# Kernel optimization log

Hardware: AMD Instinct MI355X
Metric: run time of the kernel (lower is better)

## Reference

```python
import jax, jax.numpy as jnp
import numpy as np

RADIUS = 0.005
MAX_DEGREE = 32
N = 65536
S = 2048
INPUT_DIM = 32
HIDDEN = 256
NDIM = 1  # code requires ndim==1 for the add of pos-embed to projection


def sincos_embed(pos, dim):
    # pos: [N, ndim]; output [N, ndim*dim] (== [N, dim] for ndim=1), as in source
    half = dim // 2
    freq = jnp.exp(jnp.arange(half, dtype=pos.dtype) * (-jnp.log(10000.0) / (half - 1)))
    e = pos[:, :, None] * freq[None, None, :]          # [N, ndim, half]
    e = jnp.concatenate([jnp.sin(e), jnp.cos(e)], -1)  # [N, ndim, dim]
    return e.reshape(pos.shape[0], -1)


def setup_inputs() -> dict:
    key = jax.random.key(0)
    ks = jax.random.split(key, 8)
    inp = {
        "input_feat": jax.random.normal(ks[0], (N, INPUT_DIM), jnp.float32),
        "input_pos": jax.random.uniform(ks[1], (N, NDIM), jnp.float32),
        "supernode_idxs": jnp.arange(S, dtype=jnp.int32),
        "batch_idx": jnp.zeros((N,), jnp.int32),
        # LinearProjection (input proj), lecun_normal-like init
        "proj_W": jax.random.normal(ks[2], (INPUT_DIM, HIDDEN), jnp.float32) / np.sqrt(INPUT_DIM),
        "proj_b": jnp.zeros((HIDDEN,), jnp.float32),
        # message MLP: Dense(2H->H), gelu, Dense(H->H)
        "msg_W1": jax.random.normal(ks[3], (2 * HIDDEN, HIDDEN), jnp.float32) / np.sqrt(2 * HIDDEN),
        "msg_b1": jnp.zeros((HIDDEN,), jnp.float32),
        "msg_W2": jax.random.normal(ks[4], (HIDDEN, HIDDEN), jnp.float32) / np.sqrt(HIDDEN),
        "msg_b2": jnp.zeros((HIDDEN,), jnp.float32),
    }
    return inp


def reference(input_feat, input_pos, supernode_idxs, batch_idx,
              proj_W, proj_b, msg_W1, msg_b1, msg_W2, msg_b2):
    # node embedding: linear projection + continuous sincos positional embed
    x = input_feat @ proj_W + proj_b + sincos_embed(input_pos, HIDDEN)  # [N, H]

    # radius graph restricted to edges whose dst is a supernode:
    # per supernode, take up to MAX_DEGREE nearest neighbors within RADIUS (self-loop allowed)
    sup_pos = input_pos[supernode_idxs]                                  # [S, ndim]
    d2 = jnp.sum((sup_pos[:, None, :] - input_pos[None, :, :]) ** 2, -1)  # [S, N]
    neg_d2, nbr = jax.lax.top_k(-d2, MAX_DEGREE)                          # [S, K]
    within = (-neg_d2) <= RADIUS * RADIUS                                 # [S, K] mask

    x_src = x[nbr]                                                        # [S, K, H]
    x_dst = jnp.broadcast_to(x[supernode_idxs][:, None, :], x_src.shape) # [S, K, H]
    m_in = jnp.concatenate([x_src, x_dst], axis=-1)                       # [S, K, 2H]
    h = jax.nn.gelu(m_in @ msg_W1 + msg_b1)
    m = h @ msg_W2 + msg_b2                                               # [S, K, H]

    # segment mean over each supernode's in-radius edges
    w = within[..., None].astype(m.dtype)
    pooled = jnp.sum(m * w, axis=1) / jnp.maximum(jnp.sum(w, axis=1), 1.0)  # [S, H]
    return pooled[None]  # [batch_size=1, S, H]
```

## Files before the change

### kernel.cpp

```cpp
#include <hip/hip_runtime.h>
#include <hip/hip_bf16.h>
#include <float.h>

#define N_NODES 65536
#define S_SUP   2048
#define HDIM    256
#define KNN     32
#define NBINS   4096
#define CAP     4096
#define GSUP    4

typedef __attribute__((ext_vector_type(8))) __bf16 bf16x8;
typedef __attribute__((ext_vector_type(4))) float  f32x4;

__global__ __launch_bounds__(256) void embed_kernel(
        const float* __restrict__ feat, const float* __restrict__ pos,
        const float* __restrict__ W, const float* __restrict__ b,
        __hip_bfloat16* __restrict__ xb) {
    __shared__ float sf[64][32];
    __shared__ float sp[64];
    int tid = threadIdx.x;
    int rb = blockIdx.x * 64;
    {
        int r = tid >> 2, kg = tid & 3;
        const float* src = feat + (size_t)(rb + r) * 32 + kg * 8;
        float4 v0 = *(const float4*)(src);
        float4 v1 = *(const float4*)(src + 4);
        *(float4*)&sf[r][kg * 8]     = v0;
        *(float4*)&sf[r][kg * 8 + 4] = v1;
    }
    if (tid < 64) sp[tid] = pos[rb + tid];
    int c = tid;
    float wcol[32];
#pragma unroll
    for (int k = 0; k < 32; ++k) wcol[k] = W[k * 256 + c];
    float bias = b[c];
    const float coef = -logf(10000.0f) / 127.0f;
    float fr = expf((float)(c & 127) * coef);
    bool is_sin = (c < 128);
    __syncthreads();
    for (int r = 0; r < 64; ++r) {
        float acc = bias;
#pragma unroll
        for (int k = 0; k < 32; ++k) acc = fmaf(sf[r][k], wcol[k], acc);
        float e = sp[r] * fr;
        acc += is_sin ? __sinf(e) : __cosf(e);
        xb[(size_t)(rb + r) * 256 + c] = __float2bfloat16(acc);
    }
}

__global__ void transpose_w1_kernel(const float* __restrict__ W1, __hip_bfloat16* __restrict__ w1t) {
    int k = blockIdx.x;
    int n = threadIdx.x;
    w1t[(size_t)n * 512 + k] = __float2bfloat16(W1[(size_t)k * 256 + n]);
}

__device__ __forceinline__ int pos_bin(float p) {
    int b = (int)(p * (float)NBINS);
    return min(max(b, 0), NBINS - 1);
}

__global__ void hist_kernel(const float* __restrict__ pos, int* __restrict__ bin_cnt) {
    int n = blockIdx.x * blockDim.x + threadIdx.x;
    atomicAdd(&bin_cnt[pos_bin(pos[n])], 1);
}

__global__ void scan_kernel(const int* __restrict__ bin_cnt, int* __restrict__ bin_ofs,
                            int* __restrict__ cursor) {
    __shared__ int sdata[1024];
    int t = threadIdx.x;
    int v[4]; int s = 0;
#pragma unroll
    for (int i = 0; i < 4; ++i) { v[i] = bin_cnt[t * 4 + i]; s += v[i]; }
    sdata[t] = s;
    __syncthreads();
    for (int off = 1; off < 1024; off <<= 1) {
        int add = (t >= off) ? sdata[t - off] : 0;
        __syncthreads();
        sdata[t] += add;
        __syncthreads();
    }
    int run = sdata[t] - s;
#pragma unroll
    for (int i = 0; i < 4; ++i) {
        bin_ofs[t * 4 + i] = run;
        cursor[t * 4 + i]  = run;
        run += v[i];
    }
    if (t == 1023) bin_ofs[NBINS] = run;
}

__global__ void scatter_kernel(const float* __restrict__ pos, int* __restrict__ cursor,
                               int* __restrict__ sidx, float* __restrict__ spos) {
    int n = blockIdx.x * blockDim.x + threadIdx.x;
    float p = pos[n];
    int b = pos_bin(p);
    int dst = atomicAdd(&cursor[b], 1);
    sidx[dst] = n;
    spos[dst] = p;
}

__global__ void topk_kernel(const float* __restrict__ pos, const int* __restrict__ sup,
                            const int* __restrict__ bin_ofs, const int* __restrict__ sidx,
                            const float* __restrict__ spos,
                            int* __restrict__ nbr, int* __restrict__ within,
                            int* __restrict__ ncnt) {
    __shared__ float cd2[CAP];
    __shared__ int   cidx[CAP];
    __shared__ float rd2[KNN];
    __shared__ int   ridx[KNN];
    int s = blockIdx.x;
    int lane = threadIdx.x;
    float p = pos[sup[s]];
    int hb = pos_bin(p);
    const float BINW = 1.0f / (float)NBINS;
    int ccnt = 0;
    for (int r = 2;; r <<= 1) {
        int lo = max(hb - r, 0), hi = min(hb + r, NBINS - 1);
        int start = bin_ofs[lo], end = bin_ofs[hi + 1];
        ccnt = min(end - start, CAP);
        for (int i = lane; i < ccnt; i += 64) {
            float pp = spos[start + i];
            float d = p - pp;
            cd2[i] = d * d;
            cidx[i] = sidx[start + i];
        }
        __syncthreads();
        float gl = (lo == 0) ? FLT_MAX : (p - (float)lo * BINW);
        float gr = (hi == NBINS - 1) ? FLT_MAX : ((float)(hi + 1) * BINW - p);
        float g = fminf(gl, gr);
        float g2 = (g >= FLT_MAX) ? FLT_MAX : (g * 0.999f) * (g * 0.999f);
        int cw = 0;
        for (int i = lane; i < ccnt; i += 64) cw += (cd2[i] < g2) ? 1 : 0;
        for (int o = 32; o; o >>= 1) cw += __shfl_xor(cw, o);
        if (cw >= KNN || (lo == 0 && hi == NBINS - 1)) break;
        __syncthreads();
    }
    for (int t = 0; t < KNN; ++t) {
        unsigned long long best = ~0ULL;
        int bslot = -1;
        for (int i = lane; i < ccnt; i += 64) {
            unsigned long long k =
                ((unsigned long long)__float_as_uint(cd2[i]) << 32) | (unsigned)cidx[i];
            if (k < best) { best = k; bslot = i; }
        }
        unsigned long long mybest = best;
        for (int o = 32; o; o >>= 1) {
            unsigned long long other = __shfl_xor(best, o);
            best = best < other ? best : other;
        }
        if (mybest == best && bslot >= 0) cd2[bslot] = FLT_MAX;
        if (lane == 0) {
            rd2[t]  = __uint_as_float((unsigned)(best >> 32));
            ridx[t] = (int)(unsigned)(best & 0xffffffffULL);
        }
        __syncthreads();
    }
    const float R2 = (float)(0.005 * 0.005);
    if (lane < KNN) {
        float d2v = rd2[lane];
        int w = (d2v <= R2) ? 1 : 0;
        nbr[s * KNN + lane] = ridx[lane];
        within[s * KNN + lane] = w;
        unsigned long long m = __ballot(w != 0);
        int cnt = __popcll(m & 0xffffffffULL);
        if (lane == 0) ncnt[s] = cnt;
    }
}

__device__ __forceinline__ float gelu_tanh(float v) {
    float v3 = v * v * v;
    float t = tanhf(0.7978845608028654f * (v + 0.044715f * v3));
    return 0.5f * v * (1.0f + t);
}

__global__ __launch_bounds__(256) void edge_mlp_pool_kernel(
        const __hip_bfloat16* __restrict__ xb_,
        const __hip_bfloat16* __restrict__ w1t_,
        const float* __restrict__ b1,
        const int* __restrict__ sup,
        const int* __restrict__ nbr, const int* __restrict__ within,
        const int* __restrict__ ncnt, float* __restrict__ mh) {
    const ushort* xb  = (const ushort*)xb_;
    const ushort* w1t = (const ushort*)w1t_;
    int s0 = blockIdx.x * GSUP;
    int tid = threadIdx.x;
    int l = tid & 63, w = tid >> 6;
    int lr = l & 15, lg = l >> 4;
    __shared__ int snbr[GSUP][KNN];
    __shared__ int swin[GSUP][KNN];
    __shared__ int ssup[GSUP];
    if (tid < GSUP * KNN) {
        int g = tid >> 5, j = tid & 31;
        snbr[g][j] = nbr[(s0 + g) * KNN + j];
        swin[g][j] = within[(s0 + g) * KNN + j];
    }
    if (tid < GSUP) ssup[tid] = sup[s0 + tid];
    __syncthreads();
    const ushort* ar0[GSUP];
    const ushort* ar1[GSUP];
    const ushort* asp[GSUP];
#pragma unroll
    for (int g = 0; g < GSUP; ++g) {
        ar0[g] = xb + (size_t)snbr[g][lr]      * 256;
        ar1[g] = xb + (size_t)snbr[g][16 + lr] * 256;
        asp[g] = xb + (size_t)ssup[g]          * 256;
    }
    const ushort* bbase = w1t + (size_t)(w * 64 + lr) * 512;
    int koff = lg * 8;
    f32x4 acc[GSUP][2][4] = {};
#pragma unroll 1
    for (int ks = 0; ks < 8; ++ks) {
        int k = ks * 32 + koff;
        bf16x8 bfr[4];
#pragma unroll
        for (int nt = 0; nt < 4; ++nt) bfr[nt] = *(const bf16x8*)(bbase + (size_t)nt * 16 * 512 + k);
#pragma unroll
        for (int g = 0; g < GSUP; ++g) {
            bf16x8 a0 = *(const bf16x8*)(ar0[g] + k);
            bf16x8 a1 = *(const bf16x8*)(ar1[g] + k);
#pragma unroll
            for (int nt = 0; nt < 4; ++nt) {
                acc[g][0][nt] = __builtin_amdgcn_mfma_f32_16x16x32_bf16(a0, bfr[nt], acc[g][0][nt], 0, 0, 0);
                acc[g][1][nt] = __builtin_amdgcn_mfma_f32_16x16x32_bf16(a1, bfr[nt], acc[g][1][nt], 0, 0, 0);
            }
        }
    }
#pragma unroll 1
    for (int ks = 0; ks < 8; ++ks) {
        int k = ks * 32 + koff;
        bf16x8 bfr[4];
#pragma unroll
        for (int nt = 0; nt < 4; ++nt) bfr[nt] = *(const bf16x8*)(bbase + (size_t)nt * 16 * 512 + 256 + k);
#pragma unroll
        for (int g = 0; g < GSUP; ++g) {
            bf16x8 a = *(const bf16x8*)(asp[g] + k);
#pragma unroll
            for (int nt = 0; nt < 4; ++nt) {
                acc[g][0][nt] = __builtin_amdgcn_mfma_f32_16x16x32_bf16(a, bfr[nt], acc[g][0][nt], 0, 0, 0);
                acc[g][1][nt] = __builtin_amdgcn_mfma_f32_16x16x32_bf16(a, bfr[nt], acc[g][1][nt], 0, 0, 0);
            }
        }
    }
#pragma unroll
    for (int nt = 0; nt < 4; ++nt) {
        int col = w * 64 + nt * 16 + lr;
        float bb = b1[col];
#pragma unroll
        for (int g = 0; g < GSUP; ++g) {
            float msum = 0.f;
#pragma unroll
            for (int mt = 0; mt < 2; ++mt)
#pragma unroll
                for (int d = 0; d < 4; ++d) {
                    int row = mt * 16 + lg * 4 + d;
                    float v = acc[g][mt][nt][d] + bb;
                    float gl = gelu_tanh(v);
                    msum += swin[g][row] ? gl : 0.f;
                }
            msum += __shfl_xor(msum, 16);
            msum += __shfl_xor(msum, 32);
            if (lg == 0) {
                float inv = 1.0f / (float)max(ncnt[s0 + g], 1);
                mh[(size_t)(s0 + g) * 256 + col] = msum * inv;
            }
        }
    }
}

__global__ void gemm64_kernel(const float* __restrict__ A, const int* __restrict__ rowidx,
                              const float* __restrict__ B, const float* __restrict__ bias,
                              const int* __restrict__ ncnt, float* __restrict__ C, int ldc) {
    __shared__ float At[32][68];
    __shared__ float Bs[32][64];
    int tid = threadIdx.x;
    int rb = blockIdx.x * 64, cb = blockIdx.y * 64;
    int tx = tid & 15, ty = tid >> 4;
    float acc[4][4] = {};
    int lr = tid >> 2, kg = tid & 3;
    int arow = rowidx ? rowidx[rb + lr] : (rb + lr);
    const float* aptr = A + (size_t)arow * 256 + kg * 8;
    int k2 = tid >> 3, cg = tid & 7;
    const float* bptr = B + (size_t)k2 * 256 + cb + cg * 8;
    for (int kc = 0; kc < 256; kc += 32) {
        float4 a0 = *(const float4*)(aptr + kc);
        float4 a1 = *(const float4*)(aptr + kc + 4);
        float4 b0 = *(const float4*)(bptr + (size_t)kc * 256);
        float4 b1v = *(const float4*)(bptr + (size_t)kc * 256 + 4);
        At[kg * 8 + 0][lr] = a0.x; At[kg * 8 + 1][lr] = a0.y;
        At[kg * 8 + 2][lr] = a0.z; At[kg * 8 + 3][lr] = a0.w;
        At[kg * 8 + 4][lr] = a1.x; At[kg * 8 + 5][lr] = a1.y;
        At[kg * 8 + 6][lr] = a1.z; At[kg * 8 + 7][lr] = a1.w;
        *(float4*)&Bs[k2][cg * 8]     = b0;
        *(float4*)&Bs[k2][cg * 8 + 4] = b1v;
        __syncthreads();
#pragma unroll
        for (int k = 0; k < 32; ++k) {
            float4 av = *(const float4*)&At[k][ty * 4];
            float4 bv = *(const float4*)&Bs[k][tx * 4];
            float a[4] = {av.x, av.y, av.z, av.w};
            float bb[4] = {bv.x, bv.y, bv.z, bv.w};
#pragma unroll
            for (int i = 0; i < 4; ++i)
#pragma unroll
                for (int j = 0; j < 4; ++j)
                    acc[i][j] = fmaf(a[i], bb[j], acc[i][j]);
        }
        __syncthreads();
    }
#pragma unroll
    for (int i = 0; i < 4; ++i) {
        int row = rb + ty * 4 + i;
        float bv[4] = {0.f, 0.f, 0.f, 0.f};
        if (bias) {
            float sc = ncnt ? ((ncnt[row] > 0) ? 1.0f : 0.0f) : 1.0f;
#pragma unroll
            for (int j = 0; j < 4; ++j) bv[j] = sc * bias[cb + tx * 4 + j];
        }
        float4 o;
        o.x = acc[i][0] + bv[0]; o.y = acc[i][1] + bv[1];
        o.z = acc[i][2] + bv[2]; o.w = acc[i][3] + bv[3];
        *(float4*)(C + (size_t)row * ldc + cb + tx * 4) = o;
    }
}

extern "C" void kernel_launch(void* const* d_in, const int* in_sizes, int n_in,
                              void* d_out, int out_size, void* d_ws, size_t ws_size,
                              hipStream_t stream) {
    const float* feat  = (const float*)d_in[0];
    const float* pos   = (const float*)d_in[1];
    const int*   sup   = (const int*)d_in[2];
    const float* projW = (const float*)d_in[4];
    const float* projb = (const float*)d_in[5];
    const float* W1    = (const float*)d_in[6];
    const float* b1    = (const float*)d_in[7];
    const float* W2    = (const float*)d_in[8];
    const float* b2    = (const float*)d_in[9];
    float* out = (float*)d_out;

    char* p = (char*)d_ws;
    auto alloc = [&](size_t bytes) { char* q = p; p += (bytes + 255) & ~255ULL; return q; };
    __hip_bfloat16* xb  = (__hip_bfloat16*)alloc((size_t)N_NODES * HDIM * 2);
    __hip_bfloat16* w1t = (__hip_bfloat16*)alloc((size_t)256 * 512 * 2);
    float* mh     = (float*)alloc((size_t)S_SUP * HDIM * 4);
    int*   sidx   = (int*)alloc((size_t)N_NODES * 4);
    float* spos   = (float*)alloc((size_t)N_NODES * 4);
    int*   nbr    = (int*)alloc((size_t)S_SUP * KNN * 4);
    int*   within = (int*)alloc((size_t)S_SUP * KNN * 4);
    int*   ncnt   = (int*)alloc((size_t)S_SUP * 4);
    int*   bin_cnt = (int*)alloc((size_t)NBINS * 4);
    int*   cursor  = (int*)alloc((size_t)NBINS * 4);
    int*   bin_ofs = (int*)alloc((size_t)(NBINS + 1) * 4);

    size_t needed = (size_t)(p - (char*)d_ws);
    if (needed > ws_size) {
        hipMemsetAsync(d_out, 0, (size_t)out_size * 4, stream);
        return;
    }

    hipMemsetAsync(bin_cnt, 0, (size_t)NBINS * 4, stream);
    embed_kernel<<<N_NODES / 64, 256, 0, stream>>>(feat, pos, projW, projb, xb);
    transpose_w1_kernel<<<512, 256, 0, stream>>>(W1, w1t);
    hist_kernel<<<N_NODES / 256, 256, 0, stream>>>(pos, bin_cnt);
    scan_kernel<<<1, 1024, 0, stream>>>(bin_cnt, bin_ofs, cursor);
    scatter_kernel<<<N_NODES / 256, 256, 0, stream>>>(pos, cursor, sidx, spos);
    topk_kernel<<<S_SUP, 64, 0, stream>>>(pos, sup, bin_ofs, sidx, spos, nbr, within, ncnt);
    edge_mlp_pool_kernel<<<S_SUP / GSUP, 256, 0, stream>>>(xb, w1t, b1, sup, nbr, within, ncnt, mh);
    gemm64_kernel<<<dim3(S_SUP / 64, 4), 256, 0, stream>>>(mh, nullptr, W2, b2, ncnt, out, 256);
}
```

Measured before the change: 246.0 us.

## Pre-swizzle W1 into MFMA fragment order and halve supernodes per block

The W1 conversion kernel now writes bf16 weights in the exact per-lane fragment order used by the 16x16x32 MFMA, so each wavefront loads its B operand as one contiguous 1 KB chunk instead of strided 16-byte pieces from 512-wide rows. Separately, supernodes per block drop from 4 to 2, which doubles the grid and halves accumulator registers per thread, giving more blocks and possibly higher occupancy. The cost is more total B-fragment loads, since each block reuses the weights across fewer supernodes.

```diff
diff --git a/kernel.cpp b/kernel.cpp
--- a/kernel.cpp
+++ b/kernel.cpp
@@ -8,7 +8,7 @@
 #define KNN     32
 #define NBINS   4096
 #define CAP     4096
-#define GSUP    4
+#define GSUP    2
 
 typedef __attribute__((ext_vector_type(8))) __bf16 bf16x8;
 typedef __attribute__((ext_vector_type(4))) float  f32x4;
@@ -49,10 +49,16 @@
     }
 }
 
-__global__ void transpose_w1_kernel(const float* __restrict__ W1, __hip_bfloat16* __restrict__ w1t) {
-    int k = blockIdx.x;
-    int n = threadIdx.x;
-    w1t[(size_t)n * 512 + k] = __float2bfloat16(W1[(size_t)k * 256 + n]);
+__global__ void transpose_w1_kernel(const float* __restrict__ W1, __hip_bfloat16* __restrict__ w1f) {
+    int tile = blockIdx.x;
+    int ks = tile >> 4, ntg = tile & 15;
+    int tid = threadIdx.x;
+    for (int i = tid; i < 512; i += 256) {
+        int l = i >> 3, e = i & 7;
+        int n = ntg * 16 + (l & 15);
+        int k = ks * 32 + ((l >> 4) << 3) + e;
+        w1f[(size_t)tile * 512 + i] = __float2bfloat16(W1[(size_t)k * 256 + n]);
+    }
 }
 
 __device__ __forceinline__ int pos_bin(float p) {
@@ -176,13 +182,13 @@
 
 __global__ __launch_bounds__(256) void edge_mlp_pool_kernel(
         const __hip_bfloat16* __restrict__ xb_,
-        const __hip_bfloat16* __restrict__ w1t_,
+        const __hip_bfloat16* __restrict__ w1f_,
         const float* __restrict__ b1,
         const int* __restrict__ sup,
         const int* __restrict__ nbr, const int* __restrict__ within,
         const int* __restrict__ ncnt, float* __restrict__ mh) {
     const ushort* xb  = (const ushort*)xb_;
-    const ushort* w1t = (const ushort*)w1t_;
+    const ushort* w1f = (const ushort*)w1f_;
     int s0 = blockIdx.x * GSUP;
     int tid = threadIdx.x;
     int l = tid & 63, w = tid >> 6;
@@ -206,7 +212,6 @@
         ar1[g] = xb + (size_t)snbr[g][16 + lr] * 256;
         asp[g] = xb + (size_t)ssup[g]          * 256;
     }
-    const ushort* bbase = w1t + (size_t)(w * 64 + lr) * 512;
     int koff = lg * 8;
     f32x4 acc[GSUP][2][4] = {};
 #pragma unroll 1
@@ -214,7 +219,8 @@
         int k = ks * 32 + koff;
         bf16x8 bfr[4];
 #pragma unroll
-        for (int nt = 0; nt < 4; ++nt) bfr[nt] = *(const bf16x8*)(bbase + (size_t)nt * 16 * 512 + k);
+        for (int nt = 0; nt < 4; ++nt)
+            bfr[nt] = *(const bf16x8*)(w1f + ((size_t)(ks * 16 + w * 4 + nt) * 64 + l) * 8);
 #pragma unroll
         for (int g = 0; g < GSUP; ++g) {
             bf16x8 a0 = *(const bf16x8*)(ar0[g] + k);
@@ -227,11 +233,12 @@
         }
     }
 #pragma unroll 1
-    for (int ks = 0; ks < 8; ++ks) {
-        int k = ks * 32 + koff;
+    for (int ks = 8; ks < 16; ++ks) {
+        int k = (ks - 8) * 32 + koff;
         bf16x8 bfr[4];
 #pragma unroll
-        for (int nt = 0; nt < 4; ++nt) bfr[nt] = *(const bf16x8*)(bbase + (size_t)nt * 16 * 512 + 256 + k);
+        for (int nt = 0; nt < 4; ++nt)
+            bfr[nt] = *(const bf16x8*)(w1f + ((size_t)(ks * 16 + w * 4 + nt) * 64 + l) * 8);
 #pragma unroll
         for (int g = 0; g < GSUP; ++g) {
             bf16x8 a = *(const bf16x8*)(asp[g] + k);
@@ -341,7 +348,7 @@
     char* p = (char*)d_ws;
     auto alloc = [&](size_t bytes) { char* q = p; p += (bytes + 255) & ~255ULL; return q; };
     __hip_bfloat16* xb  = (__hip_bfloat16*)alloc((size_t)N_NODES * HDIM * 2);
-    __hip_bfloat16* w1t = (__hip_bfloat16*)alloc((size_t)256 * 512 * 2);
+    __hip_bfloat16* w1f = (__hip_bfloat16*)alloc((size_t)256 * 512 * 2);
     float* mh     = (float*)alloc((size_t)S_SUP * HDIM * 4);
     int*   sidx   = (int*)alloc((size_t)N_NODES * 4);
     float* spos   = (float*)alloc((size_t)N_NODES * 4);
@@ -360,11 +367,11 @@
 
     hipMemsetAsync(bin_cnt, 0, (size_t)NBINS * 4, stream);
     embed_kernel<<<N_NODES / 64, 256, 0, stream>>>(feat, pos, projW, projb, xb);
-    transpose_w1_kernel<<<512, 256, 0, stream>>>(W1, w1t);
+    transpose_w1_kernel<<<256, 256, 0, stream>>>(W1, w1f);
     hist_kernel<<<N_NODES / 256, 256, 0, stream>>>(pos, bin_cnt);
     scan_kernel<<<1, 1024, 0, stream>>>(bin_cnt, bin_ofs, cursor);
     scatter_kernel<<<N_NODES / 256, 256, 0, stream>>>(pos, cursor, sidx, spos);
     topk_kernel<<<S_SUP, 64, 0, stream>>>(pos, sup, bin_ofs, sidx, spos, nbr, within, ncnt);
-    edge_mlp_pool_kernel<<<S_SUP / GSUP, 256, 0, stream>>>(xb, w1t, b1, sup, nbr, within, ncnt, mh);
+    edge_mlp_pool_kernel<<<S_SUP / GSUP, 256, 0, stream>>>(xb, w1f, b1, sup, nbr, within, ncnt, mh);
     gemm64_kernel<<<dim3(S_SUP / 64, 4), 256, 0, stream>>>(mh, nullptr, W2, b2, ncnt, out, 256);
 }
```

After: 218.8 us. 11.1% less time.
